# Kernel optimization log

Hardware: AMD Instinct MI355X
Metric: run time of the kernel (lower is better)

Reference implementation:

```python
import jax, jax.numpy as jnp
import numpy as np

DIM = 512
HEADS = 8
DIM_HEAD = 64
INNER = HEADS * DIM_HEAD
SCALE = DIM_HEAD ** -0.5


def setup_inputs() -> dict:
    key = jax.random.key(0)
    ks = jax.random.split(key, 6)
    x = jax.random.normal(ks[0], (8, 1024, DIM), dtype=jnp.float32)
    # nn.Linear(dim, inner, bias=False): y = x @ W.T ; store W as [out, in]
    wq = jax.random.normal(ks[1], (INNER, DIM), dtype=jnp.float32) * (DIM ** -0.5)
    wk = jax.random.normal(ks[2], (INNER, DIM), dtype=jnp.float32) * (DIM ** -0.5)
    wv = jax.random.normal(ks[3], (INNER, DIM), dtype=jnp.float32) * (DIM ** -0.5)
    wo = jax.random.normal(ks[4], (DIM, INNER), dtype=jnp.float32) * (INNER ** -0.5)
    bo = jax.random.normal(ks[5], (DIM,), dtype=jnp.float32) * 0.01
    return {"x": x, "wq": wq, "wk": wk, "wv": wv, "wo": wo, "bo": bo}


def reference(x, wq, wk, wv, wo, bo):
    b, n, _ = x.shape
    # QKV projections -> [b, h, n, d]
    def proj(w):
        return (x @ w.T).reshape(b, n, HEADS, DIM_HEAD).transpose(0, 2, 1, 3)
    q, k, v = proj(wq), proj(wk), proj(wv)
    dots = jnp.einsum('bhid,bhjd->bhij', q, k) * SCALE
    dots = jnp.clip(dots, 1e-6, 1.0)
    dots_exp = jnp.exp(dots)
    attn = dots_exp / jnp.sum(dots_exp, axis=-1, keepdims=True)
    out = jnp.einsum('bhij,bhjd->bhid', attn, v)  # [b,h,n,d]
    out = out.transpose(0, 2, 1, 3).reshape(b, n, INNER)
    return out @ wo.T + bo
```

## Files before the change

### kernel.cpp

```cpp
#include <hip/hip_runtime.h>
#include <hip/hip_fp16.h>

#define BATCH 8
#define SEQ   1024
#define DIM   512
#define HEADS 8
#define DHEAD 64
#define MTOT  (BATCH*SEQ)

typedef _Float16 f16x8 __attribute__((ext_vector_type(8)));
typedef _Float16 f16x4 __attribute__((ext_vector_type(4)));
typedef float    fx4   __attribute__((ext_vector_type(4)));

#define MFMA16 __builtin_amdgcn_mfma_f32_16x16x32_f16

__device__ __forceinline__ void gload16(const _Float16* g, _Float16* l) {
    __builtin_amdgcn_global_load_lds(
        (const __attribute__((address_space(1))) unsigned int*)g,
        (__attribute__((address_space(3))) unsigned int*)l, 16, 0, 0);
}

__global__ __launch_bounds__(256) void convert_k(
    const float* __restrict__ x,  const float* __restrict__ wq,
    const float* __restrict__ wk, const float* __restrict__ wv,
    const float* __restrict__ wo,
    _Float16* __restrict__ xb, _Float16* __restrict__ wqkvb,
    _Float16* __restrict__ wob)
{
    const int XU = (MTOT*DIM)/4;
    const int WU = (DIM*DIM)/4;
    int idx = blockIdx.x*256 + threadIdx.x;
    if (idx >= XU + 4*WU) return;
    const float* src; _Float16* dst;
    if (idx < XU) { src = x + idx*4; dst = xb + idx*4; }
    else {
        int t = idx - XU; int region = t >> 16; int off = (t & 65535)*4;
        if      (region == 0) { src = wq + off; dst = wqkvb + off; }
        else if (region == 1) { src = wk + off; dst = wqkvb + DIM*DIM + off; }
        else if (region == 2) { src = wv + off; dst = wqkvb + 2*DIM*DIM + off; }
        else                  { src = wo + off; dst = wob + off; }
    }
    float4 v = *(const float4*)src;
    f16x4 o = { (_Float16)v.x, (_Float16)v.y, (_Float16)v.z, (_Float16)v.w };
    *(f16x4*)dst = o;
}

__global__ __launch_bounds__(256,3) void qkv_proj(
    const _Float16* __restrict__ A, const _Float16* __restrict__ B,
    _Float16* __restrict__ Qb, _Float16* __restrict__ Kb,
    _Float16* __restrict__ VTb)
{
    __shared__ _Float16 lA[128*64];
    __shared__ _Float16 lB[128*64];
    const int tid = threadIdx.x;
    const int m0 = blockIdx.y*128, n0 = blockIdx.x*128;
    const int w = tid>>6, l = tid&63, lr = l&15, lq = l>>4;
    const int wr = w>>1, wc = w&1;
    const int srow = (l>>3), scol = (l&7)*8;
    fx4 acc[4][4] = {};

    for (int k0 = 0; k0 < DIM; k0 += 64) {
        __syncthreads();
#pragma unroll
        for (int t = 0; t < 4; t++) {
            int row = w*32 + t*8;
            gload16(&A[(size_t)(m0+row+srow)*DIM + k0 + scol], &lA[row*64]);
            gload16(&B[(size_t)(n0+row+srow)*DIM + k0 + scol], &lB[row*64]);
        }
        __syncthreads();
#pragma unroll
        for (int kb = 0; kb < 2; kb++) {
            f16x8 af[4], bf[4];
#pragma unroll
            for (int cb = 0; cb < 4; cb++)
                bf[cb] = *(const f16x8*)&lB[(wc*64+cb*16+lr)*64 + kb*32 + lq*8];
#pragma unroll
            for (int rb = 0; rb < 4; rb++)
                af[rb] = *(const f16x8*)&lA[(wr*64+rb*16+lr)*64 + kb*32 + lq*8];
#pragma unroll
            for (int rb = 0; rb < 4; rb++)
#pragma unroll
                for (int cb = 0; cb < 4; cb++)
                    acc[rb][cb] = MFMA16(af[rb], bf[cb], acc[rb][cb], 0,0,0);
        }
    }
    if (n0 >= 1024) {
#pragma unroll
        for (int rb = 0; rb < 4; rb++)
#pragma unroll
            for (int cb = 0; cb < 4; cb++) {
                int inner = (n0 - 1024) + wc*64 + cb*16 + lr;
                int h = inner >> 6, d = inner & 63;
                int m = m0 + wr*64 + rb*16 + lq*4;
                int b = m >> 10, n = m & 1023;
                f16x4 v4;
#pragma unroll
                for (int i = 0; i < 4; i++) v4[i] = (_Float16)acc[rb][cb][i];
                *(f16x4*)&VTb[((size_t)(b*HEADS+h)*DHEAD + d)*SEQ + n] = v4;
            }
    } else {
#pragma unroll
        for (int rb = 0; rb < 4; rb++)
#pragma unroll
            for (int cb = 0; cb < 4; cb++) {
                int nn = n0 + wc*64 + cb*16 + lr;
                int which = nn >> 9, inner = nn & 511, h = inner >> 6, d = inner & 63;
#pragma unroll
                for (int i = 0; i < 4; i++) {
                    int m = m0 + wr*64 + rb*16 + lq*4 + i;
                    int b = m >> 10, n = m & 1023;
                    float v = acc[rb][cb][i];
                    if (which == 0)
                        Qb[((b*HEADS+h)*SEQ + n)*DHEAD + d] = (_Float16)(v * 0.125f);
                    else
                        Kb[((b*HEADS+h)*SEQ + n)*DHEAD + d] = (_Float16)v;
                }
            }
    }
}

__global__ __launch_bounds__(256,4) void attn_k(
    const _Float16* __restrict__ Q, const _Float16* __restrict__ K,
    const _Float16* __restrict__ VT, _Float16* __restrict__ AO)
{
    __shared__ _Float16 lK[128*64];
    __shared__ _Float16 lVT[64*136];
    __shared__ _Float16 lPT[4][16*48];
    const int tid = threadIdx.x;
    const int w = tid>>6, l = tid&63, lr = l&15, lq = l>>4;
    const int bh = blockIdx.y, q0 = blockIdx.x*64;
    const int b = bh>>3, h = bh&7;
    const _Float16* Qp = Q  + (size_t)bh*SEQ*DHEAD;
    const _Float16* Kp = K  + (size_t)bh*SEQ*DHEAD;
    const _Float16* Vp = VT + (size_t)bh*DHEAD*SEQ;
    const int srow = (l>>3), scol = (l&7)*8;

    f16x8 qf[2];
#pragma unroll
    for (int kb = 0; kb < 2; kb++)
        qf[kb] = *(const f16x8*)&Qp[(q0 + w*16 + lr)*DHEAD + kb*32 + lq*8];

    fx4 O[4] = {};
    float lsum = 0.0f;

    for (int kt = 0; kt < 8; kt++) {
        int k0 = kt*128;
        __syncthreads();
#pragma unroll
        for (int t = 0; t < 4; t++) {
            int row = w*32 + t*8;
            gload16(&Kp[(size_t)(k0+row+srow)*DHEAD + scol], &lK[row*64]);
        }
#pragma unroll
        for (int i = 0; i < 4; i++) {
            int u = tid + i*256;
            int row = u >> 4, cu = (u & 15)*8;
            *(f16x8*)&lVT[row*136 + cu] = *(const f16x8*)&Vp[(size_t)row*SEQ + k0 + cu];
        }
        __syncthreads();

#pragma unroll
        for (int ks = 0; ks < 4; ks++) {
#pragma unroll
            for (int half = 0; half < 2; half++) {
                int rb = ks*2 + half;
                f16x8 kf0 = *(const f16x8*)&lK[(rb*16+lr)*64 + lq*8];
                f16x8 kf1 = *(const f16x8*)&lK[(rb*16+lr)*64 + 32 + lq*8];
                fx4 s = {};
                s = MFMA16(kf0, qf[0], s, 0,0,0);
                s = MFMA16(kf1, qf[1], s, 0,0,0);
                f16x4 p4;
#pragma unroll
                for (int i = 0; i < 4; i++) {
                    float p = __expf(__builtin_amdgcn_fmed3f(s[i], 1e-6f, 1.0f));
                    lsum += p;
                    p4[i] = (_Float16)p;
                }
                *(f16x4*)&lPT[w][lr*48 + half*16 + lq*4] = p4;
            }
            f16x8 pf = *(const f16x8*)&lPT[w][lr*48 + lq*8];
#pragma unroll
            for (int db = 0; db < 4; db++) {
                f16x8 vf = *(const f16x8*)&lVT[(db*16+lr)*136 + ks*32 + lq*8];
                O[db] = MFMA16(vf, pf, O[db], 0,0,0);
            }
        }
    }
    lsum += __shfl_xor(lsum, 16);
    lsum += __shfl_xor(lsum, 32);
    float inv = 1.0f / lsum;

    const int n = q0 + w*16 + lr;
    _Float16* aop = AO + ((size_t)(b*SEQ + n)*HEADS + h)*DHEAD;
#pragma unroll
    for (int db = 0; db < 4; db++) {
        f16x4 o4;
#pragma unroll
        for (int i = 0; i < 4; i++) o4[i] = (_Float16)(O[db][i] * inv);
        *(f16x4*)&aop[db*16 + lq*4] = o4;
    }
}

__global__ __launch_bounds__(256,3) void out_proj(
    const _Float16* __restrict__ A, const _Float16* __restrict__ B,
    const float* __restrict__ bo, float* __restrict__ out)
{
    __shared__ _Float16 lA[128*64];
    __shared__ _Float16 lB[128*64];
    const int tid = threadIdx.x;
    const int m0 = blockIdx.y*128, n0 = blockIdx.x*128;
    const int w = tid>>6, l = tid&63, lr = l&15, lq = l>>4;
    const int wr = w>>1, wc = w&1;
    const int srow = (l>>3), scol = (l&7)*8;
    fx4 acc[4][4] = {};

    for (int k0 = 0; k0 < DIM; k0 += 64) {
        __syncthreads();
#pragma unroll
        for (int t = 0; t < 4; t++) {
            int row = w*32 + t*8;
            gload16(&A[(size_t)(m0+row+srow)*DIM + k0 + scol], &lA[row*64]);
            gload16(&B[(size_t)(n0+row+srow)*DIM + k0 + scol], &lB[row*64]);
        }
        __syncthreads();
#pragma unroll
        for (int kb = 0; kb < 2; kb++) {
            f16x8 af[4], bf[4];
#pragma unroll
            for (int cb = 0; cb < 4; cb++)
                bf[cb] = *(const f16x8*)&lB[(wc*64+cb*16+lr)*64 + kb*32 + lq*8];
#pragma unroll
            for (int rb = 0; rb < 4; rb++)
                af[rb] = *(const f16x8*)&lA[(wr*64+rb*16+lr)*64 + kb*32 + lq*8];
#pragma unroll
            for (int rb = 0; rb < 4; rb++)
#pragma unroll
                for (int cb = 0; cb < 4; cb++)
                    acc[rb][cb] = MFMA16(af[rb], bf[cb], acc[rb][cb], 0,0,0);
        }
    }
#pragma unroll
    for (int rb = 0; rb < 4; rb++)
#pragma unroll
        for (int cb = 0; cb < 4; cb++) {
            int nn = n0 + wc*64 + cb*16 + lr;
            float bias = bo[nn];
#pragma unroll
            for (int i = 0; i < 4; i++) {
                int m = m0 + wr*64 + rb*16 + lq*4 + i;
                out[(size_t)m*DIM + nn] = acc[rb][cb][i] + bias;
            }
        }
}

extern "C" void kernel_launch(void* const* d_in, const int* in_sizes, int n_in,
                              void* d_out, int out_size, void* d_ws, size_t ws_size,
                              hipStream_t stream)
{
    const float* x  = (const float*)d_in[0];
    const float* wq = (const float*)d_in[1];
    const float* wk = (const float*)d_in[2];
    const float* wv = (const float*)d_in[3];
    const float* wo = (const float*)d_in[4];
    const float* bo = (const float*)d_in[5];
    float* out = (float*)d_out;
    char* ws = (char*)d_ws;

    _Float16* xb    = (_Float16*)(ws);
    _Float16* wqkvb = (_Float16*)(ws + 8388608);
    _Float16* wob   = (_Float16*)(ws + 9961472);
    _Float16* Qb    = (_Float16*)(ws + 10485760);
    _Float16* Kb    = (_Float16*)(ws + 18874368);
    _Float16* VTb   = (_Float16*)(ws + 27262976);
    _Float16* attnb = (_Float16*)(ws);

    convert_k<<<5120, 256, 0, stream>>>(x, wq, wk, wv, wo, xb, wqkvb, wob);
    qkv_proj<<<dim3(12, 64), 256, 0, stream>>>(xb, wqkvb, Qb, Kb, VTb);
    attn_k<<<dim3(16, 64), 256, 0, stream>>>(Qb, Kb, VTb, attnb);
    out_proj<<<dim3(4, 64), 256, 0, stream>>>(attnb, wob, bo, out);
}
```

Measured before the change: 157.7 us.

## XOR-swizzle LDS tiles in GEMMs and split attention keys across waves

```diff
diff --git a/kernel.cpp b/kernel.cpp
--- a/kernel.cpp
+++ b/kernel.cpp
@@ -56,7 +56,9 @@
     const int m0 = blockIdx.y*128, n0 = blockIdx.x*128;
     const int w = tid>>6, l = tid&63, lr = l&15, lq = l>>4;
     const int wr = w>>1, wc = w&1;
-    const int srow = (l>>3), scol = (l&7)*8;
+    const int srow = (l>>3);
+    const int scol = ((l&7) ^ ((l>>3)&7))*8;
+    const int sw = lr&7;
     fx4 acc[4][4] = {};
 
     for (int k0 = 0; k0 < DIM; k0 += 64) {
@@ -73,10 +75,10 @@
             f16x8 af[4], bf[4];
 #pragma unroll
             for (int cb = 0; cb < 4; cb++)
-                bf[cb] = *(const f16x8*)&lB[(wc*64+cb*16+lr)*64 + kb*32 + lq*8];
+                bf[cb] = *(const f16x8*)&lB[(wc*64+cb*16+lr)*64 + (((kb*4+lq)^sw))*8];
 #pragma unroll
             for (int rb = 0; rb < 4; rb++)
-                af[rb] = *(const f16x8*)&lA[(wr*64+rb*16+lr)*64 + kb*32 + lq*8];
+                af[rb] = *(const f16x8*)&lA[(wr*64+rb*16+lr)*64 + (((kb*4+lq)^sw))*8];
 #pragma unroll
             for (int rb = 0; rb < 4; rb++)
 #pragma unroll
@@ -119,85 +121,138 @@
     }
 }
 
-__global__ __launch_bounds__(256,4) void attn_k(
+__global__ __launch_bounds__(256,3) void attn_k(
     const _Float16* __restrict__ Q, const _Float16* __restrict__ K,
     const _Float16* __restrict__ VT, _Float16* __restrict__ AO)
 {
-    __shared__ _Float16 lK[128*64];
-    __shared__ _Float16 lVT[64*136];
-    __shared__ _Float16 lPT[4][16*48];
+    __shared__ __align__(16) char smem[53248];
+    _Float16* lK  = (_Float16*)smem;
+    _Float16* lVT = (_Float16*)(smem + 16384);
+    _Float16* lPT = (_Float16*)(smem + 32768);
+    _Float16* oscr = (_Float16*)smem;
+    float* lsumBuf = (float*)(smem + 32768);
+
     const int tid = threadIdx.x;
     const int w = tid>>6, l = tid&63, lr = l&15, lq = l>>4;
+    const int sw = lr&7;
     const int bh = blockIdx.y, q0 = blockIdx.x*64;
     const int b = bh>>3, h = bh&7;
     const _Float16* Qp = Q  + (size_t)bh*SEQ*DHEAD;
     const _Float16* Kp = K  + (size_t)bh*SEQ*DHEAD;
     const _Float16* Vp = VT + (size_t)bh*DHEAD*SEQ;
-    const int srow = (l>>3), scol = (l&7)*8;
-
-    f16x8 qf[2];
-#pragma unroll
-    for (int kb = 0; kb < 2; kb++)
-        qf[kb] = *(const f16x8*)&Qp[(q0 + w*16 + lr)*DHEAD + kb*32 + lq*8];
-
-    fx4 O[4] = {};
-    float lsum = 0.0f;
+    _Float16* lPw = lPT + w*2560;
+
+    const int kst_r = (l>>3), kst_c = ((l&7) ^ ((l>>3)&7))*8;
+    const int vst_r = (l>>4);
+
+    f16x8 qf[4][2];
+#pragma unroll
+    for (int qg = 0; qg < 4; qg++)
+#pragma unroll
+        for (int kb = 0; kb < 2; kb++)
+            qf[qg][kb] = *(const f16x8*)&Qp[(q0+qg*16+lr)*DHEAD + kb*32 + lq*8];
+
+    fx4 O[4][4] = {};
+    float lsum[4] = {};
 
     for (int kt = 0; kt < 8; kt++) {
         int k0 = kt*128;
         __syncthreads();
 #pragma unroll
         for (int t = 0; t < 4; t++) {
-            int row = w*32 + t*8;
-            gload16(&Kp[(size_t)(k0+row+srow)*DHEAD + scol], &lK[row*64]);
-        }
-#pragma unroll
-        for (int i = 0; i < 4; i++) {
-            int u = tid + i*256;
-            int row = u >> 4, cu = (u & 15)*8;
-            *(f16x8*)&lVT[row*136 + cu] = *(const f16x8*)&Vp[(size_t)row*SEQ + k0 + cu];
-        }
-        __syncthreads();
-
-#pragma unroll
-        for (int ks = 0; ks < 4; ks++) {
-#pragma unroll
-            for (int half = 0; half < 2; half++) {
-                int rb = ks*2 + half;
-                f16x8 kf0 = *(const f16x8*)&lK[(rb*16+lr)*64 + lq*8];
-                f16x8 kf1 = *(const f16x8*)&lK[(rb*16+lr)*64 + 32 + lq*8];
+            int rbase = w*32 + t*8;
+            gload16(&Kp[(size_t)(k0+rbase+kst_r)*DHEAD + kst_c], &lK[rbase*64]);
+        }
+#pragma unroll
+        for (int t = 0; t < 4; t++) {
+            int rbase = w*16 + t*4;
+            int r = rbase + vst_r;
+            int g = (l&15) ^ (r&7);
+            gload16(&Vp[(size_t)r*SEQ + k0 + g*8], &lVT[rbase*128]);
+        }
+        __syncthreads();
+
+#pragma unroll
+        for (int rb2 = 0; rb2 < 2; rb2++) {
+            int jrow = w*32 + rb2*16 + lr;
+            f16x8 kf0 = *(const f16x8*)&lK[jrow*64 + ((lq^sw))*8];
+            f16x8 kf1 = *(const f16x8*)&lK[jrow*64 + (((4+lq)^sw))*8];
+#pragma unroll
+            for (int qg = 0; qg < 4; qg++) {
                 fx4 s = {};
-                s = MFMA16(kf0, qf[0], s, 0,0,0);
-                s = MFMA16(kf1, qf[1], s, 0,0,0);
+                s = MFMA16(kf0, qf[qg][0], s, 0,0,0);
+                s = MFMA16(kf1, qf[qg][1], s, 0,0,0);
                 f16x4 p4;
 #pragma unroll
                 for (int i = 0; i < 4; i++) {
                     float p = __expf(__builtin_amdgcn_fmed3f(s[i], 1e-6f, 1.0f));
-                    lsum += p;
+                    lsum[qg] += p;
                     p4[i] = (_Float16)p;
                 }
-                *(f16x4*)&lPT[w][lr*48 + half*16 + lq*4] = p4;
-            }
-            f16x8 pf = *(const f16x8*)&lPT[w][lr*48 + lq*8];
+                *(f16x4*)&lPw[(qg*16+lr)*40 + rb2*16 + lq*4] = p4;
+            }
+        }
+        f16x8 vf[4];
+#pragma unroll
+        for (int db = 0; db < 4; db++)
+            vf[db] = *(const f16x8*)&lVT[(db*16+lr)*128 + (((w*4+lq)^sw))*8];
+#pragma unroll
+        for (int qg = 0; qg < 4; qg++) {
+            f16x8 pf = *(const f16x8*)&lPw[(qg*16+lr)*40 + lq*8];
+#pragma unroll
+            for (int db = 0; db < 4; db++)
+                O[db][qg] = MFMA16(vf[db], pf, O[db][qg], 0,0,0);
+        }
+    }
+
+#pragma unroll
+    for (int qg = 0; qg < 4; qg++) {
+        lsum[qg] += __shfl_xor(lsum[qg], 16);
+        lsum[qg] += __shfl_xor(lsum[qg], 32);
+    }
+    __syncthreads();
+    if (lq == 0) {
+#pragma unroll
+        for (int qg = 0; qg < 4; qg++)
+            lsumBuf[w*64 + qg*16 + lr] = lsum[qg];
+    }
+    if (w > 0) {
+        _Float16* oo = oscr + (w-1)*4352;
+#pragma unroll
+        for (int db = 0; db < 4; db++)
+#pragma unroll
+            for (int qg = 0; qg < 4; qg++) {
+                f16x4 t;
+#pragma unroll
+                for (int i = 0; i < 4; i++) t[i] = (_Float16)O[db][qg][i];
+                *(f16x4*)&oo[(qg*16+lr)*68 + db*16 + lq*4] = t;
+            }
+    }
+    __syncthreads();
+    if (w == 0) {
+#pragma unroll
+        for (int qg = 0; qg < 4; qg++) {
+            float tot = lsum[qg] + lsumBuf[64 + qg*16+lr]
+                      + lsumBuf[128 + qg*16+lr] + lsumBuf[192 + qg*16+lr];
+            float inv = 1.0f / tot;
+            int q = q0 + qg*16 + lr;
+            _Float16* aop = AO + ((size_t)(b*SEQ + q)*HEADS + h)*DHEAD;
 #pragma unroll
             for (int db = 0; db < 4; db++) {
-                f16x8 vf = *(const f16x8*)&lVT[(db*16+lr)*136 + ks*32 + lq*8];
-                O[db] = MFMA16(vf, pf, O[db], 0,0,0);
-            }
-        }
-    }
-    lsum += __shfl_xor(lsum, 16);
-    lsum += __shfl_xor(lsum, 32);
-    float inv = 1.0f / lsum;
-
-    const int n = q0 + w*16 + lr;
-    _Float16* aop = AO + ((size_t)(b*SEQ + n)*HEADS + h)*DHEAD;
-#pragma unroll
-    for (int db = 0; db < 4; db++) {
-        f16x4 o4;
-#pragma unroll
-        for (int i = 0; i < 4; i++) o4[i] = (_Float16)(O[db][i] * inv);
-        *(f16x4*)&aop[db*16 + lq*4] = o4;
+                fx4 o = O[db][qg];
+#pragma unroll
+                for (int ww = 1; ww < 4; ww++) {
+                    f16x4 t = *(const f16x4*)
+                        &oscr[(ww-1)*4352 + (qg*16+lr)*68 + db*16 + lq*4];
+#pragma unroll
+                    for (int i = 0; i < 4; i++) o[i] += (float)t[i];
+                }
+                f16x4 r;
+#pragma unroll
+                for (int i = 0; i < 4; i++) r[i] = (_Float16)(o[i] * inv);
+                *(f16x4*)&aop[db*16 + lq*4] = r;
+            }
+        }
     }
 }
 
@@ -211,7 +266,9 @@
     const int m0 = blockIdx.y*128, n0 = blockIdx.x*128;
     const int w = tid>>6, l = tid&63, lr = l&15, lq = l>>4;
     const int wr = w>>1, wc = w&1;
-    const int srow = (l>>3), scol = (l&7)*8;
+    const int srow = (l>>3);
+    const int scol = ((l&7) ^ ((l>>3)&7))*8;
+    const int sw = lr&7;
     fx4 acc[4][4] = {};
 
     for (int k0 = 0; k0 < DIM; k0 += 64) {
@@ -228,10 +285,10 @@
             f16x8 af[4], bf[4];
 #pragma unroll
             for (int cb = 0; cb < 4; cb++)
-                bf[cb] = *(const f16x8*)&lB[(wc*64+cb*16+lr)*64 + kb*32 + lq*8];
+                bf[cb] = *(const f16x8*)&lB[(wc*64+cb*16+lr)*64 + (((kb*4+lq)^sw))*8];
 #pragma unroll
             for (int rb = 0; rb < 4; rb++)
-                af[rb] = *(const f16x8*)&lA[(wr*64+rb*16+lr)*64 + kb*32 + lq*8];
+                af[rb] = *(const f16x8*)&lA[(wr*64+rb*16+lr)*64 + (((kb*4+lq)^sw))*8];
 #pragma unroll
             for (int rb = 0; rb < 4; rb++)
 #pragma unroll
```

Measured after the change: 153.0 us. 1.03x faster.
